# Kernel optimization log

Measured on AMD Instinct MI355X. Metric: run time of the kernel, lower is better.

Reference implementation:

```python
import jax, jax.numpy as jnp
import numpy as np
import math

B, S, H, NH, DK, K = 256, 200, 768, 12, 64, 64
EPS = 1e-12

def setup_inputs() -> dict:
    key = jax.random.key(0)
    ks = jax.random.split(key, 8)
    sc = 0.02
    return {
        "x": jax.random.normal(ks[0], (B, S, H), dtype=jnp.float32),
        "mask": jnp.ones((B, 1, S), dtype=jnp.float32),
        "Wq": jax.random.normal(ks[1], (H, H), dtype=jnp.float32) * sc,
        "bq": jnp.zeros((H,), dtype=jnp.float32),
        "Wk": jax.random.normal(ks[2], (H, H), dtype=jnp.float32) * sc,
        "bk": jnp.zeros((H,), dtype=jnp.float32),
        "Wv": jax.random.normal(ks[3], (H, H), dtype=jnp.float32) * sc,
        "bv": jnp.zeros((H,), dtype=jnp.float32),
        "We": jax.random.normal(ks[4], (K, S), dtype=jnp.float32) * sc,
        "be": jnp.zeros((K,), dtype=jnp.float32),
        "Wf": jax.random.normal(ks[5], (K, S), dtype=jnp.float32) * sc,
        "bf": jnp.zeros((K,), dtype=jnp.float32),
        "Wd": jax.random.normal(ks[6], (H, H), dtype=jnp.float32) * sc,
        "bd": jnp.zeros((H,), dtype=jnp.float32),
        "gamma": jnp.ones((H,), dtype=jnp.float32),
        "beta": jnp.zeros((H,), dtype=jnp.float32),
    }

def _heads(t):  # [B,S,H] -> [B,NH,S,DK]
    return t.reshape(B, S, NH, DK).transpose(0, 2, 1, 3)

def reference(x, mask, Wq, bq, Wk, bk, Wv, bv, We, be, Wf, bf, Wd, bd, gamma, beta):
    q = _heads(x @ Wq.T + bq)
    k = _heads(x @ Wk.T + bk)
    v = _heads(x @ Wv.T + bv)
    m = mask[:, 0:1, :, None]            # [B,1,S,1]
    k = k * m
    v = v * m
    # Linformer seq projections: E on value, F on key (applied along seq axis)
    v = jnp.einsum("bhsd,ks->bhkd", v, We) + be[:, None]   # [B,NH,K,DK]
    k = jnp.einsum("bhsd,ks->bhkd", k, Wf) + bf[:, None]   # [B,NH,K,DK]
    scores = jnp.einsum("bhqd,bhkd->bhqk", q, k) / math.sqrt(DK)
    p_attn = jax.nn.softmax(scores, axis=-1)               # [B,NH,S,K]
    ctx = jnp.einsum("bhqk,bhkd->bhqd", p_attn, v)         # [B,NH,S,DK]
    ctx = ctx.transpose(0, 2, 1, 3).reshape(B, S, H)
    h = ctx @ Wd.T + bd + x                                # dense + residual (dropout=0)
    mu = jnp.mean(h, axis=-1, keepdims=True)
    var = jnp.mean(jnp.square(h - mu), axis=-1, keepdims=True)
    out = (h - mu) / jnp.sqrt(var + EPS) * gamma + beta
    return out, p_attn
```

## Files before the change

kernel.cpp:

```cpp
#include <hip/hip_runtime.h>
#include <stdint.h>

typedef unsigned short u16;
typedef short bf16x8 __attribute__((ext_vector_type(8)));
typedef float f32x4 __attribute__((ext_vector_type(4)));

#define NB   256
#define NS   200
#define NHID 768
#define NHEAD 12
#define NDK  64
#define NK   64
#define NBH  (NB*NHEAD)
#define NM   (NB*NS)
#define SP   224

__device__ __forceinline__ u16 f2b(float f){
  unsigned u = __builtin_bit_cast(unsigned, f);
  return (u16)((u + 0x7FFFu + ((u>>16)&1u)) >> 16);
}
__device__ __forceinline__ bf16x8 pack8(const float* v){
  bf16x8 r;
#pragma unroll
  for (int i=0;i<8;i++) r[i] = (short)f2b(v[i]);
  return r;
}
__device__ __forceinline__ f32x4 mfma16(bf16x8 a, bf16x8 b, f32x4 c){
  return __builtin_amdgcn_mfma_f32_16x16x32_bf16(a, b, c, 0, 0, 0);
}
__device__ __forceinline__ void gload16(u16* l, const u16* g){
  __builtin_amdgcn_global_load_lds(
      (const __attribute__((address_space(1))) void*)g,
      (__attribute__((address_space(3))) void*)l, 16, 0, 0);
}

__global__ __launch_bounds__(256) void pack_w(
    const float* __restrict__ Wq, const float* __restrict__ Wk,
    const float* __restrict__ Wv, const float* __restrict__ Wd,
    u16* __restrict__ Wqb, u16* __restrict__ Wkb,
    u16* __restrict__ Wvb, u16* __restrict__ Wdb)
{
  const int i = blockIdx.x*256 + threadIdx.x;
  Wqb[i]=f2b(Wq[i]); Wkb[i]=f2b(Wk[i]); Wvb[i]=f2b(Wv[i]); Wdb[i]=f2b(Wd[i]);
}

__global__ __launch_bounds__(256) void pack_wfe(
    const float* __restrict__ Wf, const float* __restrict__ We, u16* __restrict__ Wfeb)
{
  const int r = blockIdx.x, s = threadIdx.x;
  if (s < SP){
    float v = 0.f;
    if (s < NS) v = (r<64) ? Wf[r*NS+s] : We[(r-64)*NS+s];
    Wfeb[r*SP+s] = f2b(v);
  }
}

__global__ __launch_bounds__(128) void rowsums_k(
    const float* __restrict__ Wf, const float* __restrict__ We,
    const float* __restrict__ mask, float* __restrict__ rs)
{
  const int b = blockIdx.x, kk = threadIdx.x;
  const float* src = (kk<64) ? (Wf + kk*NS) : (We + (kk-64)*NS);
  float acc = 0.f;
  for (int s=0;s<NS;s++) acc += src[s]*mask[b*NS+s];
  rs[b*128+kk] = acc;
}

__global__ __launch_bounds__(256) void transpose_x(
    const float* __restrict__ x, const float* __restrict__ mask,
    u16* __restrict__ xb, u16* __restrict__ xbT)
{
  __shared__ u16 LT[64*232];
  const int t = threadIdx.x, b = blockIdx.x, n0 = blockIdx.y*64;
  for (int i=0;i<50;i++){
    const int idx = i*256 + t;
    const int s = idx>>6, n = idx&63;
    const size_t gi = ((size_t)b*NS + s)*NHID + n0 + n;
    const float v = x[gi];
    xb[gi] = f2b(v);
    const float mv = mask[b*NS+s];
    LT[n*232 + s] = f2b(v*mv);
  }
  __syncthreads();
  const int row = t>>2, cb = t&3;
  u16* dst = xbT + (size_t)b*NHID*SP + (size_t)(n0+row)*SP;
  for (int i=0;i<7;i++){
    const int c = cb + i*4;
    bf16x8 vv = (c<25) ? *(const bf16x8*)&LT[row*232 + c*8] : (bf16x8)0;
    *(bf16x8*)&dst[c*8] = vv;
  }
}

__global__ __launch_bounds__(256) void gemm_yfe(
    const u16* __restrict__ Wfeb, const u16* __restrict__ xbT, u16* __restrict__ yfe)
{
  __shared__ u16 Al[128*64];
  __shared__ u16 Bl[128*64];
  const int t=threadIdx.x, w=t>>6, lane=t&63, hi=lane>>4, lo=lane&15;
  const int sr=lane>>3, sc=lane&7;
  const int b=blockIdx.x, col0=blockIdx.y*128;
  const u16* Bg = xbT + (size_t)b*NHID*SP;
  f32x4 acc[4][4];
#pragma unroll
  for(int i=0;i<4;i++)
#pragma unroll
    for(int j=0;j<4;j++) acc[i][j]=(f32x4)0.0f;
  const u16* Ab=&Al[((w>>1)*64+lo)*64 + hi*8];
  const u16* Bb=&Bl[((w&1)*64+lo)*64 + hi*8];

  for (int kt=0; kt<192; kt+=64){
#pragma unroll
    for (int i8=0;i8<4;i8++){
      const int r = w*32 + i8*8 + sr;
      gload16(&Al[r*64 + sc*8], Wfeb + (size_t)r*SP + kt + sc*8);
      gload16(&Bl[r*64 + sc*8], Bg + (size_t)(col0+r)*SP + kt + sc*8);
    }
    asm volatile("s_waitcnt vmcnt(0)" ::: "memory");
    __syncthreads();
#pragma unroll
    for (int ks=0; ks<2; ks++){
      bf16x8 a[4], bfr[4];
#pragma unroll
      for (int i=0;i<4;i++) a[i]   = *(const bf16x8*)(Ab + i*16*64 + ks*32);
#pragma unroll
      for (int j=0;j<4;j++) bfr[j] = *(const bf16x8*)(Bb + j*16*64 + ks*32);
#pragma unroll
      for (int i=0;i<4;i++)
#pragma unroll
        for (int j=0;j<4;j++) acc[i][j] = mfma16(a[i], bfr[j], acc[i][j]);
    }
    __syncthreads();
  }
#pragma unroll
  for (int i8=0;i8<2;i8++){
    const int r2 = w*32 + i8*16 + (lane>>2);
    gload16(&Al[r2*32 + (lane&3)*8], Wfeb + (size_t)r2*SP + 192 + (lane&3)*8);
    gload16(&Bl[r2*32 + (lane&3)*8], Bg + (size_t)(col0+r2)*SP + 192 + (lane&3)*8);
  }
  asm volatile("s_waitcnt vmcnt(0)" ::: "memory");
  __syncthreads();
  {
    bf16x8 a[4], bfr[4];
#pragma unroll
    for (int i=0;i<4;i++) a[i]   = *(const bf16x8*)&Al[((w>>1)*64+i*16+lo)*32 + hi*8];
#pragma unroll
    for (int j=0;j<4;j++) bfr[j] = *(const bf16x8*)&Bl[((w&1)*64+j*16+lo)*32 + hi*8];
#pragma unroll
    for (int i=0;i<4;i++)
#pragma unroll
      for (int j=0;j<4;j++) acc[i][j] = mfma16(a[i], bfr[j], acc[i][j]);
  }
  const int mbase=(w>>1)*64, nbase=col0+(w&1)*64;
#pragma unroll
  for (int i=0;i<4;i++)
#pragma unroll
    for (int r=0;r<4;r++){
      const int m = mbase + i*16 + hi*4 + r;
#pragma unroll
      for (int j=0;j<4;j++){
        const int n = nbase + j*16 + lo;
        yfe[(size_t)b*98304 + (size_t)m*NHID + n] = f2b(acc[i][j][r]);
      }
    }
}

template<int EPI>
__global__ __launch_bounds__(512, 2) void gemm_ring(
    const u16* __restrict__ Ag_, const u16* __restrict__ Bg_,
    const float* __restrict__ bias, const float* __restrict__ resid,
    void* __restrict__ Cout)
{
  __shared__ u16 AS[4][8192];
  __shared__ u16 BS[4][8192];
  const int t = threadIdx.x;
  const int w = t>>6, lane = t&63, hi = lane>>4, lo = lane&15;
  const int wm = w>>2, wn = w&3;
  const int row0 = blockIdx.x*256, col0 = blockIdx.y*256;
  const u16* Ag = Ag_ + (size_t)row0*NHID;
  const u16* Bg = Bg_ + (size_t)col0*NHID;
  const int rp0 = t>>3, cc = t&7;

  f32x4 acc[8][4];
#pragma unroll
  for (int i=0;i<8;i++)
#pragma unroll
    for (int j=0;j<4;j++) acc[i][j] = (f32x4)0.0f;

  int aoff[8], boff[4];
#pragma unroll
  for (int i=0;i<8;i++){
    const int r = wm*128 + i*16 + lo;
    const int rp = r>>1, c = (r&1)*4 + hi;
    aoff[i] = rp*64 + ((c ^ (rp&7))<<3);
  }
#pragma unroll
  for (int j=0;j<4;j++){
    const int n = wn*64 + j*16 + lo;
    const int rp = n>>1, c = (n&1)*4 + hi;
    boff[j] = rp*64 + ((c ^ (rp&7))<<3);
  }

  auto stage = [&](int s, int kt){
#pragma unroll
    for (int i8=0;i8<2;i8++){
      const int rp = i8*64 + rp0;
      const int c  = cc ^ (rp&7);
      const int grow = rp*2 + (c>>2);
      const int gcol = (c&3)<<3;
      gload16(&AS[s][rp*64 + cc*8], Ag + (size_t)grow*NHID + kt + gcol);
      gload16(&BS[s][rp*64 + cc*8], Bg + (size_t)grow*NHID + kt + gcol);
    }
  };
  auto body = [&](const u16* as_, const u16* bs_){
    bf16x8 av[8], bvv[4];
#pragma unroll
    for (int j=0;j<4;j++) bvv[j] = *(const bf16x8*)(bs_ + boff[j]);
#pragma unroll
    for (int i=0;i<8;i++) av[i] = *(const bf16x8*)(as_ + aoff[i]);
    __builtin_amdgcn_s_setprio(1);
#pragma unroll
    for (int i=0;i<8;i++)
#pragma unroll
      for (int j=0;j<4;j++) acc[i][j] = mfma16(av[i], bvv[j], acc[i][j]);
    __builtin_amdgcn_s_setprio(0);
  };
  auto step = [&](int tt, int s){
    if (tt+3 < 24) stage((s+3)&3, (tt+3)*32);
    body(AS[s], BS[s]);
    if (tt <= 20)      { asm volatile("s_waitcnt vmcnt(8)" ::: "memory"); }
    else if (tt == 21) { asm volatile("s_waitcnt vmcnt(4)" ::: "memory"); }
    else if (tt == 22) { asm volatile("s_waitcnt vmcnt(0)" ::: "memory"); }
    if (tt < 23){
      __builtin_amdgcn_sched_barrier(0);
      asm volatile("s_barrier" ::: "memory");
      __builtin_amdgcn_sched_barrier(0);
    }
  };

  stage(0,0); stage(1,32); stage(2,64);
  asm volatile("s_waitcnt vmcnt(8)" ::: "memory");
  asm volatile("s_barrier" ::: "memory");
  __builtin_amdgcn_sched_barrier(0);

#pragma unroll
  for (int tt=0; tt<24; tt+=4){
    step(tt,0); step(tt+1,1); step(tt+2,2); step(tt+3,3);
  }

#pragma unroll
  for (int i=0;i<8;i++)
#pragma unroll
    for (int q=0;q<4;q++){
      const int m = row0 + wm*128 + i*16 + hi*4 + q;
#pragma unroll
      for (int j=0;j<4;j++){
        const int n = col0 + wn*64 + j*16 + lo;
        const float v = acc[i][j][q] + bias[n];
        if constexpr (EPI==0){
          const int b = m/NS, s = m - b*NS;
          ((u16*)Cout)[(((size_t)b*NHEAD + (n>>6))*NS + s)*NDK + (n&63)] = f2b(v);
        } else {
          const size_t gi = (size_t)m*NHID + n;
          ((float*)Cout)[gi] = v + resid[gi];
        }
      }
    }
}

__global__ __launch_bounds__(256) void gemm_kproj(
    const u16* __restrict__ yfe, const u16* __restrict__ Wkb,
    const float* __restrict__ rs, const float* __restrict__ bk,
    const float* __restrict__ bff, u16* __restrict__ kproj)
{
  __shared__ u16 Al[64*64];
  __shared__ u16 Bl[128*64];
  const int t=threadIdx.x, w=t>>6, lane=t&63, hi=lane>>4, lo=lane&15;
  const int sr=lane>>3, sc=lane&7;
  const int b=blockIdx.x, col0=blockIdx.y*128;
  const u16* yf = yfe + (size_t)b*98304;
  f32x4 acc[2][4];
#pragma unroll
  for(int i=0;i<2;i++)
#pragma unroll
    for(int j=0;j<4;j++) acc[i][j]=(f32x4)0.0f;
  const u16* Ab=&Al[((w>>1)*32+lo)*64 + hi*8];
  const u16* Bb=&Bl[((w&1)*64+lo)*64 + hi*8];

  for (int kt=0; kt<NHID; kt+=64){
#pragma unroll
    for (int i8=0;i8<2;i8++){
      const int r = w*16 + i8*8 + sr;
      gload16(&Al[r*64 + sc*8], yf + (size_t)r*NHID + kt + sc*8);
    }
#pragma unroll
    for (int i8=0;i8<4;i8++){
      const int r = w*32 + i8*8 + sr;
      gload16(&Bl[r*64 + sc*8], Wkb + (size_t)(col0+r)*NHID + kt + sc*8);
    }
    asm volatile("s_waitcnt vmcnt(0)" ::: "memory");
    __syncthreads();
#pragma unroll
    for (int ks=0; ks<2; ks++){
      bf16x8 a[2], bfr[4];
#pragma unroll
      for (int i=0;i<2;i++) a[i]   = *(const bf16x8*)(Ab + i*16*64 + ks*32);
#pragma unroll
      for (int j=0;j<4;j++) bfr[j] = *(const bf16x8*)(Bb + j*16*64 + ks*32);
#pragma unroll
      for (int i=0;i<2;i++)
#pragma unroll
        for (int j=0;j<4;j++) acc[i][j] = mfma16(a[i], bfr[j], acc[i][j]);
    }
    __syncthreads();
  }
  const int mbase=(w>>1)*32, nbase=col0+(w&1)*64;
#pragma unroll
  for (int i=0;i<2;i++)
#pragma unroll
    for (int r=0;r<4;r++){
      const int m = mbase + i*16 + hi*4 + r;
      const float rsv = rs[b*128 + m], bfv = bff[m];
#pragma unroll
      for (int j=0;j<4;j++){
        const int n = nbase + j*16 + lo;
        kproj[(size_t)b*49152 + (size_t)m*NHID + n] = f2b(acc[i][j][r] + rsv*bk[n] + bfv);
      }
    }
}

__global__ __launch_bounds__(256) void gemm_vprojT(
    const u16* yfe, const u16* __restrict__ Wvb,
    const float* __restrict__ rs, const float* __restrict__ bv,
    const float* __restrict__ bee, u16* vout)
{
  __shared__ u16 Al[128*64];
  __shared__ u16 Bl[64*64];
  const int t=threadIdx.x, w=t>>6, lane=t&63, hi=lane>>4, lo=lane&15;
  const int sr=lane>>3, sc=lane&7;
  const int b=blockIdx.x, row0=blockIdx.y*128;
  const u16* ye = yfe + (size_t)b*98304 + 49152;
  f32x4 acc[4][2];
#pragma unroll
  for(int i=0;i<4;i++)
#pragma unroll
    for(int j=0;j<2;j++) acc[i][j]=(f32x4)0.0f;
  const u16* Ab=&Al[((w>>1)*64+lo)*64 + hi*8];
  const u16* Bb=&Bl[((w&1)*32+lo)*64 + hi*8];

  for (int kt=0; kt<NHID; kt+=64){
#pragma unroll
    for (int i8=0;i8<4;i8++){
      const int r = w*32 + i8*8 + sr;
      gload16(&Al[r*64 + sc*8], Wvb + (size_t)(row0+r)*NHID + kt + sc*8);
    }
#pragma unroll
    for (int i8=0;i8<2;i8++){
      const int r = w*16 + i8*8 + sr;
      gload16(&Bl[r*64 + sc*8], ye + (size_t)r*NHID + kt + sc*8);
    }
    asm volatile("s_waitcnt vmcnt(0)" ::: "memory");
    __syncthreads();
#pragma unroll
    for (int ks=0; ks<2; ks++){
      bf16x8 a[4], bfr[2];
#pragma unroll
      for (int i=0;i<4;i++) a[i]   = *(const bf16x8*)(Ab + i*16*64 + ks*32);
#pragma unroll
      for (int j=0;j<2;j++) bfr[j] = *(const bf16x8*)(Bb + j*16*64 + ks*32);
#pragma unroll
      for (int i=0;i<4;i++)
#pragma unroll
        for (int j=0;j<2;j++) acc[i][j] = mfma16(a[i], bfr[j], acc[i][j]);
    }
    __syncthreads();
  }
  const int mbase=row0+(w>>1)*64, nbase=(w&1)*32;
#pragma unroll
  for (int i=0;i<4;i++)
#pragma unroll
    for (int r=0;r<4;r++){
      const int m = mbase + i*16 + hi*4 + r;
      const float bvv = bv[m];
#pragma unroll
      for (int j=0;j<2;j++){
        const int n = nbase + j*16 + lo;
        vout[(size_t)b*98304 + (size_t)m*64 + n] = f2b(acc[i][j][r] + rs[b*128+64+n]*bvv + bee[n]);
      }
    }
}

__global__ __launch_bounds__(256) void attn_kernel(
    const u16* __restrict__ qb,
    const u16* __restrict__ kproj,
    const u16* __restrict__ vprojT,
    float* __restrict__ pout,
    u16* __restrict__ ctxb)
{
  __shared__ u16 QL[208*72];
  __shared__ u16 KP[64*72];
  __shared__ u16 VP[64*72];
  const int t=threadIdx.x, w=t>>6, lane=t&63, hi=lane>>4, lo=lane&15;
  const int bh = blockIdx.x, b=bh/NHEAD, hh=bh%NHEAD;
  for (int c=t;c<1600;c+=256){
    const int row=c>>3, col8=(c&7)*8;
    *(bf16x8*)&QL[row*72+col8] = *(const bf16x8*)(qb + (size_t)bh*12800 + c*8);
  }
  if (t<72){ const int row=200+t/9, col8=(t%9)*8; *(bf16x8*)&QL[row*72+col8]=(bf16x8)0; }
  for (int c=t;c<512;c+=256){
    const int row=c>>3, col8=(c&7)*8;
    *(bf16x8*)&KP[row*72+col8] = *(const bf16x8*)(kproj  + (size_t)b*49152 + (size_t)row*NHID + hh*64 + col8);
    *(bf16x8*)&VP[row*72+col8] = *(const bf16x8*)(vprojT + (size_t)b*98304 + (size_t)(hh*64+row)*64 + col8);
  }
  __syncthreads();
  const int mf0 = (w==0)?0:(1+w*3);
  const int nmf = (w==0)?4:3;
  f32x4 acc[4][4];
#pragma unroll
  for(int i=0;i<4;i++)
#pragma unroll
    for(int j=0;j<4;j++) acc[i][j]=(f32x4)0.0f;
#pragma unroll
  for (int ks=0; ks<2; ks++){
    bf16x8 a[4], bb[4];
#pragma unroll
    for (int j=0;j<4;j++) bb[j]=*(const bf16x8*)&KP[(j*16+lo)*72 + ks*32 + hi*8];
#pragma unroll
    for (int i=0;i<4;i++) if (i<nmf) a[i]=*(const bf16x8*)&QL[((mf0+i)*16+lo)*72 + ks*32 + hi*8];
#pragma unroll
    for (int i=0;i<4;i++) if (i<nmf)
#pragma unroll
      for (int j=0;j<4;j++)
        acc[i][j]=mfma16(a[i],bb[j],acc[i][j]);
  }
  __syncthreads();

#pragma unroll
  for (int i=0;i<4;i++) if (i<nmf){
#pragma unroll
    for (int r=0;r<4;r++){
      const int q = (mf0+i)*16 + hi*4 + r;
      float s0=acc[i][0][r]*0.125f, s1=acc[i][1][r]*0.125f,
            s2=acc[i][2][r]*0.125f, s3=acc[i][3][r]*0.125f;
      float mx=fmaxf(fmaxf(s0,s1),fmaxf(s2,s3));
      mx=fmaxf(mx,__shfl_xor(mx,1)); mx=fmaxf(mx,__shfl_xor(mx,2));
      mx=fmaxf(mx,__shfl_xor(mx,4)); mx=fmaxf(mx,__shfl_xor(mx,8));
      float e0=__expf(s0-mx), e1=__expf(s1-mx), e2=__expf(s2-mx), e3=__expf(s3-mx);
      float sm=e0+e1+e2+e3;
      sm+=__shfl_xor(sm,1); sm+=__shfl_xor(sm,2); sm+=__shfl_xor(sm,4); sm+=__shfl_xor(sm,8);
      const float inv=1.0f/sm;
      const float p0=e0*inv,p1=e1*inv,p2=e2*inv,p3=e3*inv;
      if (q<NS){
        float* pg = pout + ((size_t)bh*NS + q)*NK + lo;
        pg[0]=p0; pg[16]=p1; pg[32]=p2; pg[48]=p3;
      }
      u16* pl = &QL[q*72 + lo];
      pl[0]=f2b(p0); pl[16]=f2b(p1); pl[32]=f2b(p2); pl[48]=f2b(p3);
    }
  }
  f32x4 acc2[4][4];
#pragma unroll
  for(int i=0;i<4;i++)
#pragma unroll
    for(int j=0;j<4;j++) acc2[i][j]=(f32x4)0.0f;
#pragma unroll
  for (int ks=0; ks<2; ks++){
    bf16x8 a[4], bb[4];
#pragma unroll
    for (int j=0;j<4;j++) bb[j]=*(const bf16x8*)&VP[(j*16+lo)*72 + ks*32 + hi*8];
#pragma unroll
    for (int i=0;i<4;i++) if (i<nmf) a[i]=*(const bf16x8*)&QL[((mf0+i)*16+lo)*72 + ks*32 + hi*8];
#pragma unroll
    for (int i=0;i<4;i++) if (i<nmf)
#pragma unroll
      for (int j=0;j<4;j++)
        acc2[i][j]=mfma16(a[i],bb[j],acc2[i][j]);
  }
#pragma unroll
  for (int i=0;i<4;i++) if (i<nmf)
#pragma unroll
    for (int r=0;r<4;r++){
      const int q=(mf0+i)*16+hi*4+r;
      if (q<NS){
#pragma unroll
        for (int j=0;j<4;j++){
          const int d=j*16+lo;
          ctxb[((size_t)b*NS+q)*NHID + hh*NDK + d] = f2b(acc2[i][j][r]);
        }
      }
    }
}

__global__ __launch_bounds__(192) void ln_kernel(
    float* __restrict__ out, const float* __restrict__ gamma, const float* __restrict__ beta)
{
  __shared__ float ps[3], pq[3];
  const int t = threadIdx.x;
  float4* row = (float4*)(out + (size_t)blockIdx.x*NHID);
  float4 v = row[t];
  float s = v.x+v.y+v.z+v.w;
  float q = v.x*v.x + v.y*v.y + v.z*v.z + v.w*v.w;
#pragma unroll
  for (int m=1;m<64;m<<=1){ s += __shfl_xor(s,m); q += __shfl_xor(q,m); }
  if ((t&63)==0){ ps[t>>6]=s; pq[t>>6]=q; }
  __syncthreads();
  s = ps[0]+ps[1]+ps[2]; q = pq[0]+pq[1]+pq[2];
  const float mu = s*(1.0f/768.0f);
  const float var = q*(1.0f/768.0f) - mu*mu;
  const float rs = rsqrtf(var + 1e-12f);
  const float4 g  = ((const float4*)gamma)[t];
  const float4 be = ((const float4*)beta)[t];
  float4 o;
  o.x=(v.x-mu)*rs*g.x+be.x; o.y=(v.y-mu)*rs*g.y+be.y;
  o.z=(v.z-mu)*rs*g.z+be.z; o.w=(v.w-mu)*rs*g.w+be.w;
  row[t]=o;
}

extern "C" void kernel_launch(void* const* d_in, const int* in_sizes, int n_in,
                              void* d_out, int out_size, void* d_ws, size_t ws_size,
                              hipStream_t stream)
{
  (void)in_sizes; (void)n_in; (void)out_size; (void)ws_size;
  const float* x    = (const float*)d_in[0];
  const float* mask = (const float*)d_in[1];
  const float* Wq   = (const float*)d_in[2];
  const float* bq   = (const float*)d_in[3];
  const float* Wk   = (const float*)d_in[4];
  const float* bk   = (const float*)d_in[5];
  const float* Wv   = (const float*)d_in[6];
  const float* bv   = (const float*)d_in[7];
  const float* We   = (const float*)d_in[8];
  const float* be   = (const float*)d_in[9];
  const float* Wf   = (const float*)d_in[10];
  const float* bf   = (const float*)d_in[11];
  const float* Wd   = (const float*)d_in[12];
  const float* bd   = (const float*)d_in[13];
  const float* gamma= (const float*)d_in[14];
  const float* beta = (const float*)d_in[15];

  float* out  = (float*)d_out;
  float* pout = out + (size_t)NM*NHID;

  char* ws = (char*)d_ws;
  u16* xb    = (u16*)(ws);
  u16* ctxb  = (u16*)(ws);
  u16* xbT   = (u16*)(ws + 78643200ull);
  u16* qb    = (u16*)(ws + 78643200ull);
  u16* yfe   = (u16*)(ws + 166723584ull);
  u16* vprojT= (u16*)(ws + 166723584ull);
  u16* kproj = (u16*)(ws + 217055232ull);
  u16* Wqb   = (u16*)(ws + 242221056ull);
  u16* Wkb   = (u16*)(ws + 243400704ull);
  u16* Wvb   = (u16*)(ws + 244580352ull);
  u16* Wdb   = (u16*)(ws + 245760000ull);
  u16* Wfeb  = (u16*)(ws + 246939648ull);
  float* rsb = (float*)(ws + 246996992ull);

  pack_w  <<<2304,256,0,stream>>>(Wq,Wk,Wv,Wd,Wqb,Wkb,Wvb,Wdb);
  pack_wfe<<<128, 256,0,stream>>>(Wf,We,Wfeb);
  rowsums_k<<<NB, 128,0,stream>>>(Wf,We,mask,rsb);
  transpose_x<<<dim3(NB,12),256,0,stream>>>(x,mask,xb,xbT);
  gemm_yfe<<<dim3(NB,6),256,0,stream>>>(Wfeb,xbT,yfe);
  gemm_ring<0><<<dim3(200,3),512,0,stream>>>(xb,Wqb,bq,nullptr,qb);
  gemm_kproj <<<dim3(NB,6),256,0,stream>>>(yfe,Wkb,rsb,bk,bf,kproj);
  gemm_vprojT<<<dim3(NB,6),256,0,stream>>>(yfe,Wvb,rsb,bv,be,vprojT);
  attn_kernel<<<NBH,256,0,stream>>>(qb,kproj,vprojT,pout,ctxb);
  gemm_ring<1><<<dim3(200,3),512,0,stream>>>(ctxb,Wdb,bd,x,out);
  ln_kernel<<<NM,192,0,stream>>>(out,gamma,beta);
}
```

Measured before the change: 588.5 us.

## Merge prep and K/V projection kernels, store pre-LN output as bf16

The three weight-prep kernels become one launch, and the K and V projection GEMMs become a single grid with a z dimension, which cuts launch count and lets the two projections overlap. The dense GEMM epilogue now reads the bf16 copy of x as the residual and writes h as bf16 instead of fp32, shrinking that intermediate's traffic. A new LayerNorm kernel uses one wave per row in a grid-stride loop and reads bf16 input. This lowers precision on the residual and pre-norm values, and the workspace layout moves so that V, ctx and h get separate regions.

```diff
diff --git a/kernel.cpp b/kernel.cpp
--- a/kernel.cpp
+++ b/kernel.cpp
@@ -4,6 +4,7 @@
 typedef unsigned short u16;
 typedef short bf16x8 __attribute__((ext_vector_type(8)));
 typedef float f32x4 __attribute__((ext_vector_type(4)));
+typedef unsigned short u16x4 __attribute__((ext_vector_type(4)));
 
 #define NB   256
 #define NS   200
@@ -19,11 +20,8 @@
   unsigned u = __builtin_bit_cast(unsigned, f);
   return (u16)((u + 0x7FFFu + ((u>>16)&1u)) >> 16);
 }
-__device__ __forceinline__ bf16x8 pack8(const float* v){
-  bf16x8 r;
-#pragma unroll
-  for (int i=0;i<8;i++) r[i] = (short)f2b(v[i]);
-  return r;
+__device__ __forceinline__ float b2f(u16 b){
+  return __builtin_bit_cast(float, (unsigned)b << 16);
 }
 __device__ __forceinline__ f32x4 mfma16(bf16x8 a, bf16x8 b, f32x4 c){
   return __builtin_amdgcn_mfma_f32_16x16x32_bf16(a, b, c, 0, 0, 0);
@@ -34,36 +32,30 @@
       (__attribute__((address_space(3))) void*)l, 16, 0, 0);
 }
 
-__global__ __launch_bounds__(256) void pack_w(
+__global__ __launch_bounds__(256) void prep_kernel(
     const float* __restrict__ Wq, const float* __restrict__ Wk,
     const float* __restrict__ Wv, const float* __restrict__ Wd,
+    const float* __restrict__ Wf, const float* __restrict__ We,
+    const float* __restrict__ mask,
     u16* __restrict__ Wqb, u16* __restrict__ Wkb,
-    u16* __restrict__ Wvb, u16* __restrict__ Wdb)
-{
-  const int i = blockIdx.x*256 + threadIdx.x;
+    u16* __restrict__ Wvb, u16* __restrict__ Wdb,
+    u16* __restrict__ Wfeb, float* __restrict__ rs)
+{
+  const int blk = blockIdx.x, t = threadIdx.x;
+  const int i = blk*256 + t;
   Wqb[i]=f2b(Wq[i]); Wkb[i]=f2b(Wk[i]); Wvb[i]=f2b(Wv[i]); Wdb[i]=f2b(Wd[i]);
-}
-
-__global__ __launch_bounds__(256) void pack_wfe(
-    const float* __restrict__ Wf, const float* __restrict__ We, u16* __restrict__ Wfeb)
-{
-  const int r = blockIdx.x, s = threadIdx.x;
-  if (s < SP){
+  if (blk < 128 && t < SP){
     float v = 0.f;
-    if (s < NS) v = (r<64) ? Wf[r*NS+s] : We[(r-64)*NS+s];
-    Wfeb[r*SP+s] = f2b(v);
-  }
-}
-
-__global__ __launch_bounds__(128) void rowsums_k(
-    const float* __restrict__ Wf, const float* __restrict__ We,
-    const float* __restrict__ mask, float* __restrict__ rs)
-{
-  const int b = blockIdx.x, kk = threadIdx.x;
-  const float* src = (kk<64) ? (Wf + kk*NS) : (We + (kk-64)*NS);
-  float acc = 0.f;
-  for (int s=0;s<NS;s++) acc += src[s]*mask[b*NS+s];
-  rs[b*128+kk] = acc;
+    if (t < NS) v = (blk<64) ? Wf[blk*NS+t] : We[(blk-64)*NS+t];
+    Wfeb[blk*SP+t] = f2b(v);
+  }
+  if (blk >= 1024 && blk < 1280 && t < 128){
+    const int b = blk-1024;
+    const float* src = (t<64) ? (Wf + t*NS) : (We + (t-64)*NS);
+    float acc = 0.f;
+    for (int s=0;s<NS;s++) acc += src[s]*mask[b*NS+s];
+    rs[b*128+t] = acc;
+  }
 }
 
 __global__ __launch_bounds__(256) void transpose_x(
@@ -167,8 +159,8 @@
 template<int EPI>
 __global__ __launch_bounds__(512, 2) void gemm_ring(
     const u16* __restrict__ Ag_, const u16* __restrict__ Bg_,
-    const float* __restrict__ bias, const float* __restrict__ resid,
-    void* __restrict__ Cout)
+    const float* __restrict__ bias, const u16* __restrict__ resid,
+    u16* __restrict__ Cout)
 {
   __shared__ u16 AS[4][8192];
   __shared__ u16 BS[4][8192];
@@ -255,138 +247,135 @@
 #pragma unroll
       for (int j=0;j<4;j++){
         const int n = col0 + wn*64 + j*16 + lo;
-        const float v = acc[i][j][q] + bias[n];
+        float v = acc[i][j][q] + bias[n];
         if constexpr (EPI==0){
           const int b = m/NS, s = m - b*NS;
-          ((u16*)Cout)[(((size_t)b*NHEAD + (n>>6))*NS + s)*NDK + (n&63)] = f2b(v);
+          Cout[(((size_t)b*NHEAD + (n>>6))*NS + s)*NDK + (n&63)] = f2b(v);
         } else {
           const size_t gi = (size_t)m*NHID + n;
-          ((float*)Cout)[gi] = v + resid[gi];
+          Cout[gi] = f2b(v + b2f(resid[gi]));
         }
       }
     }
 }
 
-__global__ __launch_bounds__(256) void gemm_kproj(
+__global__ __launch_bounds__(256) void gemm_projkv(
     const u16* __restrict__ yfe, const u16* __restrict__ Wkb,
-    const float* __restrict__ rs, const float* __restrict__ bk,
-    const float* __restrict__ bff, u16* __restrict__ kproj)
-{
-  __shared__ u16 Al[64*64];
-  __shared__ u16 Bl[128*64];
+    const u16* __restrict__ Wvb, const float* __restrict__ rs,
+    const float* __restrict__ bk, const float* __restrict__ bv,
+    const float* __restrict__ bff, const float* __restrict__ bee,
+    u16* __restrict__ kproj, u16* __restrict__ vout)
+{
+  __shared__ u16 S[192*64];
   const int t=threadIdx.x, w=t>>6, lane=t&63, hi=lane>>4, lo=lane&15;
   const int sr=lane>>3, sc=lane&7;
-  const int b=blockIdx.x, col0=blockIdx.y*128;
-  const u16* yf = yfe + (size_t)b*98304;
-  f32x4 acc[2][4];
-#pragma unroll
-  for(int i=0;i<2;i++)
-#pragma unroll
-    for(int j=0;j<4;j++) acc[i][j]=(f32x4)0.0f;
-  const u16* Ab=&Al[((w>>1)*32+lo)*64 + hi*8];
-  const u16* Bb=&Bl[((w&1)*64+lo)*64 + hi*8];
-
-  for (int kt=0; kt<NHID; kt+=64){
-#pragma unroll
-    for (int i8=0;i8<2;i8++){
-      const int r = w*16 + i8*8 + sr;
-      gload16(&Al[r*64 + sc*8], yf + (size_t)r*NHID + kt + sc*8);
-    }
-#pragma unroll
-    for (int i8=0;i8<4;i8++){
-      const int r = w*32 + i8*8 + sr;
-      gload16(&Bl[r*64 + sc*8], Wkb + (size_t)(col0+r)*NHID + kt + sc*8);
-    }
-    asm volatile("s_waitcnt vmcnt(0)" ::: "memory");
-    __syncthreads();
-#pragma unroll
-    for (int ks=0; ks<2; ks++){
-      bf16x8 a[2], bfr[4];
-#pragma unroll
-      for (int i=0;i<2;i++) a[i]   = *(const bf16x8*)(Ab + i*16*64 + ks*32);
-#pragma unroll
-      for (int j=0;j<4;j++) bfr[j] = *(const bf16x8*)(Bb + j*16*64 + ks*32);
-#pragma unroll
-      for (int i=0;i<2;i++)
-#pragma unroll
-        for (int j=0;j<4;j++) acc[i][j] = mfma16(a[i], bfr[j], acc[i][j]);
-    }
-    __syncthreads();
-  }
-  const int mbase=(w>>1)*32, nbase=col0+(w&1)*64;
-#pragma unroll
-  for (int i=0;i<2;i++)
-#pragma unroll
-    for (int r=0;r<4;r++){
-      const int m = mbase + i*16 + hi*4 + r;
-      const float rsv = rs[b*128 + m], bfv = bff[m];
-#pragma unroll
-      for (int j=0;j<4;j++){
-        const int n = nbase + j*16 + lo;
-        kproj[(size_t)b*49152 + (size_t)m*NHID + n] = f2b(acc[i][j][r] + rsv*bk[n] + bfv);
-      }
-    }
-}
-
-__global__ __launch_bounds__(256) void gemm_vprojT(
-    const u16* yfe, const u16* __restrict__ Wvb,
-    const float* __restrict__ rs, const float* __restrict__ bv,
-    const float* __restrict__ bee, u16* vout)
-{
-  __shared__ u16 Al[128*64];
-  __shared__ u16 Bl[64*64];
-  const int t=threadIdx.x, w=t>>6, lane=t&63, hi=lane>>4, lo=lane&15;
-  const int sr=lane>>3, sc=lane&7;
-  const int b=blockIdx.x, row0=blockIdx.y*128;
-  const u16* ye = yfe + (size_t)b*98304 + 49152;
-  f32x4 acc[4][2];
-#pragma unroll
-  for(int i=0;i<4;i++)
-#pragma unroll
-    for(int j=0;j<2;j++) acc[i][j]=(f32x4)0.0f;
-  const u16* Ab=&Al[((w>>1)*64+lo)*64 + hi*8];
-  const u16* Bb=&Bl[((w&1)*32+lo)*64 + hi*8];
-
-  for (int kt=0; kt<NHID; kt+=64){
-#pragma unroll
-    for (int i8=0;i8<4;i8++){
-      const int r = w*32 + i8*8 + sr;
-      gload16(&Al[r*64 + sc*8], Wvb + (size_t)(row0+r)*NHID + kt + sc*8);
-    }
-#pragma unroll
-    for (int i8=0;i8<2;i8++){
-      const int r = w*16 + i8*8 + sr;
-      gload16(&Bl[r*64 + sc*8], ye + (size_t)r*NHID + kt + sc*8);
-    }
-    asm volatile("s_waitcnt vmcnt(0)" ::: "memory");
-    __syncthreads();
-#pragma unroll
-    for (int ks=0; ks<2; ks++){
-      bf16x8 a[4], bfr[2];
-#pragma unroll
-      for (int i=0;i<4;i++) a[i]   = *(const bf16x8*)(Ab + i*16*64 + ks*32);
-#pragma unroll
-      for (int j=0;j<2;j++) bfr[j] = *(const bf16x8*)(Bb + j*16*64 + ks*32);
-#pragma unroll
-      for (int i=0;i<4;i++)
-#pragma unroll
-        for (int j=0;j<2;j++) acc[i][j] = mfma16(a[i], bfr[j], acc[i][j]);
-    }
-    __syncthreads();
-  }
-  const int mbase=row0+(w>>1)*64, nbase=(w&1)*32;
-#pragma unroll
-  for (int i=0;i<4;i++)
-#pragma unroll
-    for (int r=0;r<4;r++){
-      const int m = mbase + i*16 + hi*4 + r;
-      const float bvv = bv[m];
-#pragma unroll
-      for (int j=0;j<2;j++){
-        const int n = nbase + j*16 + lo;
-        vout[(size_t)b*98304 + (size_t)m*64 + n] = f2b(acc[i][j][r] + rs[b*128+64+n]*bvv + bee[n]);
-      }
-    }
+  const int b=blockIdx.x;
+
+  if (blockIdx.z==0){
+    u16* Al = S;
+    u16* Bl = S + 64*64;
+    const int col0=blockIdx.y*128;
+    const u16* yf = yfe + (size_t)b*98304;
+    f32x4 acc[2][4];
+#pragma unroll
+    for(int i=0;i<2;i++)
+#pragma unroll
+      for(int j=0;j<4;j++) acc[i][j]=(f32x4)0.0f;
+    const u16* Ab=&Al[((w>>1)*32+lo)*64 + hi*8];
+    const u16* Bb=&Bl[((w&1)*64+lo)*64 + hi*8];
+    for (int kt=0; kt<NHID; kt+=64){
+#pragma unroll
+      for (int i8=0;i8<2;i8++){
+        const int r = w*16 + i8*8 + sr;
+        gload16(&Al[r*64 + sc*8], yf + (size_t)r*NHID + kt + sc*8);
+      }
+#pragma unroll
+      for (int i8=0;i8<4;i8++){
+        const int r = w*32 + i8*8 + sr;
+        gload16(&Bl[r*64 + sc*8], Wkb + (size_t)(col0+r)*NHID + kt + sc*8);
+      }
+      asm volatile("s_waitcnt vmcnt(0)" ::: "memory");
+      __syncthreads();
+#pragma unroll
+      for (int ks=0; ks<2; ks++){
+        bf16x8 a[2], bfr[4];
+#pragma unroll
+        for (int i=0;i<2;i++) a[i]   = *(const bf16x8*)(Ab + i*16*64 + ks*32);
+#pragma unroll
+        for (int j=0;j<4;j++) bfr[j] = *(const bf16x8*)(Bb + j*16*64 + ks*32);
+#pragma unroll
+        for (int i=0;i<2;i++)
+#pragma unroll
+          for (int j=0;j<4;j++) acc[i][j] = mfma16(a[i], bfr[j], acc[i][j]);
+      }
+      __syncthreads();
+    }
+    const int mbase=(w>>1)*32, nbase=col0+(w&1)*64;
+#pragma unroll
+    for (int i=0;i<2;i++)
+#pragma unroll
+      for (int r=0;r<4;r++){
+        const int m = mbase + i*16 + hi*4 + r;
+        const float rsv = rs[b*128 + m], bfv = bff[m];
+#pragma unroll
+        for (int j=0;j<4;j++){
+          const int n = nbase + j*16 + lo;
+          kproj[(size_t)b*49152 + (size_t)m*NHID + n] = f2b(acc[i][j][r] + rsv*bk[n] + bfv);
+        }
+      }
+  } else {
+    u16* Al = S;
+    u16* Bl = S + 128*64;
+    const int row0=blockIdx.y*128;
+    const u16* ye = yfe + (size_t)b*98304 + 49152;
+    f32x4 acc[4][2];
+#pragma unroll
+    for(int i=0;i<4;i++)
+#pragma unroll
+      for(int j=0;j<2;j++) acc[i][j]=(f32x4)0.0f;
+    const u16* Ab=&Al[((w>>1)*64+lo)*64 + hi*8];
+    const u16* Bb=&Bl[((w&1)*32+lo)*64 + hi*8];
+    for (int kt=0; kt<NHID; kt+=64){
+#pragma unroll
+      for (int i8=0;i8<4;i8++){
+        const int r = w*32 + i8*8 + sr;
+        gload16(&Al[r*64 + sc*8], Wvb + (size_t)(row0+r)*NHID + kt + sc*8);
+      }
+#pragma unroll
+      for (int i8=0;i8<2;i8++){
+        const int r = w*16 + i8*8 + sr;
+        gload16(&Bl[r*64 + sc*8], ye + (size_t)r*NHID + kt + sc*8);
+      }
+      asm volatile("s_waitcnt vmcnt(0)" ::: "memory");
+      __syncthreads();
+#pragma unroll
+      for (int ks=0; ks<2; ks++){
+        bf16x8 a[4], bfr[2];
+#pragma unroll
+        for (int i=0;i<4;i++) a[i]   = *(const bf16x8*)(Ab + i*16*64 + ks*32);
+#pragma unroll
+        for (int j=0;j<2;j++) bfr[j] = *(const bf16x8*)(Bb + j*16*64 + ks*32);
+#pragma unroll
+        for (int i=0;i<4;i++)
+#pragma unroll
+          for (int j=0;j<2;j++) acc[i][j] = mfma16(a[i], bfr[j], acc[i][j]);
+      }
+      __syncthreads();
+    }
+    const int mbase=row0+(w>>1)*64, nbase=(w&1)*32;
+#pragma unroll
+    for (int i=0;i<4;i++)
+#pragma unroll
+      for (int r=0;r<4;r++){
+        const int m = mbase + i*16 + hi*4 + r;
+        const float bvv = bv[m];
+#pragma unroll
+        for (int j=0;j<2;j++){
+          const int n = nbase + j*16 + lo;
+          vout[(size_t)b*49152 + (size_t)m*64 + n] = f2b(acc[i][j][r] + rs[b*128+64+n]*bvv + bee[n]);
+        }
+      }
+  }
 }
 
 __global__ __launch_bounds__(256) void attn_kernel(
@@ -409,7 +398,7 @@
   for (int c=t;c<512;c+=256){
     const int row=c>>3, col8=(c&7)*8;
     *(bf16x8*)&KP[row*72+col8] = *(const bf16x8*)(kproj  + (size_t)b*49152 + (size_t)row*NHID + hh*64 + col8);
-    *(bf16x8*)&VP[row*72+col8] = *(const bf16x8*)(vprojT + (size_t)b*98304 + (size_t)(hh*64+row)*64 + col8);
+    *(bf16x8*)&VP[row*72+col8] = *(const bf16x8*)(vprojT + (size_t)b*49152 + (size_t)(hh*64+row)*64 + col8);
   }
   __syncthreads();
   const int mf0 = (w==0)?0:(1+w*3);
@@ -490,29 +479,42 @@
     }
 }
 
-__global__ __launch_bounds__(192) void ln_kernel(
-    float* __restrict__ out, const float* __restrict__ gamma, const float* __restrict__ beta)
-{
-  __shared__ float ps[3], pq[3];
-  const int t = threadIdx.x;
-  float4* row = (float4*)(out + (size_t)blockIdx.x*NHID);
-  float4 v = row[t];
-  float s = v.x+v.y+v.z+v.w;
-  float q = v.x*v.x + v.y*v.y + v.z*v.z + v.w*v.w;
-#pragma unroll
-  for (int m=1;m<64;m<<=1){ s += __shfl_xor(s,m); q += __shfl_xor(q,m); }
-  if ((t&63)==0){ ps[t>>6]=s; pq[t>>6]=q; }
-  __syncthreads();
-  s = ps[0]+ps[1]+ps[2]; q = pq[0]+pq[1]+pq[2];
-  const float mu = s*(1.0f/768.0f);
-  const float var = q*(1.0f/768.0f) - mu*mu;
-  const float rs = rsqrtf(var + 1e-12f);
-  const float4 g  = ((const float4*)gamma)[t];
-  const float4 be = ((const float4*)beta)[t];
-  float4 o;
-  o.x=(v.x-mu)*rs*g.x+be.x; o.y=(v.y-mu)*rs*g.y+be.y;
-  o.z=(v.z-mu)*rs*g.z+be.z; o.w=(v.w-mu)*rs*g.w+be.w;
-  row[t]=o;
+__global__ __launch_bounds__(256) void ln2_kernel(
+    const u16* __restrict__ h, const float* __restrict__ gamma,
+    const float* __restrict__ beta, float* __restrict__ outp)
+{
+  const int t = threadIdx.x, wid = t>>6, lane = t&63;
+  float g_[12], be_[12];
+#pragma unroll
+  for (int k=0;k<3;k++){
+    float4 gg = *(const float4*)(gamma + lane*12 + k*4);
+    float4 bb = *(const float4*)(beta  + lane*12 + k*4);
+    g_[k*4+0]=gg.x; g_[k*4+1]=gg.y; g_[k*4+2]=gg.z; g_[k*4+3]=gg.w;
+    be_[k*4+0]=bb.x; be_[k*4+1]=bb.y; be_[k*4+2]=bb.z; be_[k*4+3]=bb.w;
+  }
+  for (int row = blockIdx.x*4 + wid; row < NM; row += 1600*4){
+    const u16* hr = h + (size_t)row*NHID + lane*12;
+    u16x4 a0 = *(const u16x4*)hr;
+    u16x4 a1 = *(const u16x4*)(hr+4);
+    u16x4 a2 = *(const u16x4*)(hr+8);
+    float v[12];
+#pragma unroll
+    for (int k=0;k<4;k++){
+      v[k]   = b2f(a0[k]);
+      v[4+k] = b2f(a1[k]);
+      v[8+k] = b2f(a2[k]);
+    }
+    float s=0.f, q=0.f;
+#pragma unroll
+    for (int k=0;k<12;k++){ s+=v[k]; q+=v[k]*v[k]; }
+#pragma unroll
+    for (int m=1;m<64;m<<=1){ s+=__shfl_xor(s,m); q+=__shfl_xor(q,m); }
+    const float mu = s*(1.0f/768.0f);
+    const float rsv = rsqrtf(q*(1.0f/768.0f) - mu*mu + 1e-12f);
+    float* orow = outp + (size_t)row*NHID + lane*12;
+#pragma unroll
+    for (int k=0;k<12;k++) orow[k] = (v[k]-mu)*rsv*g_[k] + be_[k];
+  }
 }
 
 extern "C" void kernel_launch(void* const* d_in, const int* in_sizes, int n_in,
@@ -542,11 +544,9 @@
 
   char* ws = (char*)d_ws;
   u16* xb    = (u16*)(ws);
-  u16* ctxb  = (u16*)(ws);
   u16* xbT   = (u16*)(ws + 78643200ull);
   u16* qb    = (u16*)(ws + 78643200ull);
   u16* yfe   = (u16*)(ws + 166723584ull);
-  u16* vprojT= (u16*)(ws + 166723584ull);
   u16* kproj = (u16*)(ws + 217055232ull);
   u16* Wqb   = (u16*)(ws + 242221056ull);
   u16* Wkb   = (u16*)(ws + 243400704ull);
@@ -554,16 +554,16 @@
   u16* Wdb   = (u16*)(ws + 245760000ull);
   u16* Wfeb  = (u16*)(ws + 246939648ull);
   float* rsb = (float*)(ws + 246996992ull);
-
-  pack_w  <<<2304,256,0,stream>>>(Wq,Wk,Wv,Wd,Wqb,Wkb,Wvb,Wdb);
-  pack_wfe<<<128, 256,0,stream>>>(Wf,We,Wfeb);
-  rowsums_k<<<NB, 128,0,stream>>>(Wf,We,mask,rsb);
+  u16* vprojT= (u16*)(ws + 247128064ull);
+  u16* ctxb  = (u16*)(ws + 272293888ull);
+  u16* hb    = (u16*)(ws + 350937088ull);
+
+  prep_kernel<<<2304,256,0,stream>>>(Wq,Wk,Wv,Wd,Wf,We,mask,Wqb,Wkb,Wvb,Wdb,Wfeb,rsb);
   transpose_x<<<dim3(NB,12),256,0,stream>>>(x,mask,xb,xbT);
   gemm_yfe<<<dim3(NB,6),256,0,stream>>>(Wfeb,xbT,yfe);
   gemm_ring<0><<<dim3(200,3),512,0,stream>>>(xb,Wqb,bq,nullptr,qb);
-  gemm_kproj <<<dim3(NB,6),256,0,stream>>>(yfe,Wkb,rsb,bk,bf,kproj);
-  gemm_vprojT<<<dim3(NB,6),256,0,stream>>>(yfe,Wvb,rsb,bv,be,vprojT);
+  gemm_projkv<<<dim3(NB,6,2),256,0,stream>>>(yfe,Wkb,Wvb,rsb,bk,bv,bf,be,kproj,vprojT);
   attn_kernel<<<NBH,256,0,stream>>>(qb,kproj,vprojT,pout,ctxb);
-  gemm_ring<1><<<dim3(200,3),512,0,stream>>>(ctxb,Wdb,bd,x,out);
-  ln_kernel<<<NM,192,0,stream>>>(out,gamma,beta);
-}
+  gemm_ring<1><<<dim3(200,3),512,0,stream>>>(ctxb,Wdb,bd,xb,hb);
+  ln2_kernel<<<1600,256,0,stream>>>(hb,gamma,beta,out);
+}
```

New measurement: 568.0 us. -3.5%, faster.
